# Performance work log

Hardware: AMD Instinct MI355X
Metric: run time of the kernel (lower is better)

Reference implementation:

```python
import jax, jax.numpy as jnp
import numpy as np

D_IN_NUM = 16
D_IN_CAT = 16
D_OUT = 10
DIM = 512
N_FREQ = 32
FREQ_SCALE = 0.01
D_EMB = 48
TEMP = 1.0
CHUNK = 5000


def setup_inputs() -> dict:
    key = jax.random.key(0)
    ks = jax.random.split(key, 10)
    B, N = 1024, 40000
    d_in_total = D_IN_NUM * D_EMB + D_IN_CAT
    return {
        "x_num": jax.random.uniform(ks[0], (B, D_IN_NUM), dtype=jnp.float32),
        "x_cat": jax.random.uniform(ks[1], (B, D_IN_CAT), dtype=jnp.float32),
        "y": jax.random.randint(ks[2], (B,), 0, D_OUT),
        "candidate_x_num": jax.random.uniform(ks[3], (N, D_IN_NUM), dtype=jnp.float32),
        "candidate_x_cat": jax.random.uniform(ks[4], (N, D_IN_CAT), dtype=jnp.float32),
        "candidate_y": jax.random.randint(ks[5], (N,), 0, D_OUT),
        "frequencies": FREQ_SCALE * jax.random.normal(ks[6], (D_IN_NUM, N_FREQ), dtype=jnp.float32),
        "lin_w": 0.05 * jax.random.normal(ks[7], (2 * N_FREQ, D_EMB), dtype=jnp.float32),
        "lin_b": jnp.zeros((D_EMB,), dtype=jnp.float32),
        "enc_w": 0.02 * jax.random.normal(ks[8], (d_in_total, DIM), dtype=jnp.float32),
        "enc_b": jnp.zeros((DIM,), dtype=jnp.float32),
    }


def _plr_encode(x_num, x_cat, frequencies, lin_w, lin_b, enc_w, enc_b):
    # PLR 'lite' embedding: [B, F] -> [B, F, 2*n_freq] -> [B, F, d_emb]
    t = 2.0 * jnp.pi * frequencies[None] * x_num[:, :, None]        # [B,F,n_freq]
    feats = jnp.concatenate([jnp.cos(t), jnp.sin(t)], axis=-1)       # [B,F,2n_freq]
    emb = jax.nn.relu(feats @ lin_w + lin_b)                         # [B,F,d_emb]
    flat = emb.reshape(emb.shape[0], -1)                             # [B,F*d_emb]
    h = jnp.concatenate([flat, x_cat], axis=1) @ enc_w + enc_b       # [B,dim]
    return h


def reference(x_num, x_cat, y, candidate_x_num, candidate_x_cat, candidate_y,
              frequencies, lin_w, lin_b, enc_w, enc_b):
    q = _plr_encode(x_num, x_cat, frequencies, lin_w, lin_b, enc_w, enc_b)           # [B,dim]
    c = _plr_encode(candidate_x_num, candidate_x_cat, frequencies, lin_w, lin_b, enc_w, enc_b)  # [N,dim]
    cand_y = jax.nn.one_hot(candidate_y, D_OUT, dtype=jnp.float32)                   # [N,K]

    # pairwise Euclidean distance (matmul form, as torch.cdist)
    d2 = (jnp.sum(q * q, axis=1, keepdims=True)
          + jnp.sum(c * c, axis=1)[None, :]
          - 2.0 * q @ c.T)
    dist = jnp.sqrt(jnp.maximum(d2, 1e-12)) / TEMP                                   # [B,N]
    exp_d = jnp.exp(-dist)                                                           # [B,N]

    # original accumulates per-5000-chunk logsumexp of exp(-d) additively
    B, N = exp_d.shape
    n_chunks = N // CHUNK
    lse = jax.nn.logsumexp(exp_d.reshape(B, n_chunks, CHUNK), axis=-1).sum(axis=-1)  # [B]
    logits = exp_d @ cand_y                                                          # [B,K]
    return jnp.log(logits) - lse[:, None]
```

## Files before the change

kernel.cpp:

```cpp
#include <hip/hip_runtime.h>
#include <math.h>

typedef __attribute__((ext_vector_type(8))) short bf16x8;
typedef __attribute__((ext_vector_type(4))) float f32x4;
typedef unsigned short u16;
typedef unsigned int u32;

#define BQ 1024
#define NCAND 40000
#define ROWS_TOT 41024
#define NF 16
#define NFREQ 32
#define DEMB 48
#define KDIM 800
#define ASTRIDE 808
#define DIM 512
#define NCLS 10
#define NCHUNK 8
#define CHUNKSZ 5000
#define CT_PER_CHUNK 40
#define NCT 320
#define PSTRIDE 136
#define MROWS 64
#define TWO_PI 6.28318530717958647692f

__device__ __forceinline__ u16 f2bf(float f) {
  u32 u = __float_as_uint(f);
  u32 r = u + 0x7fffu + ((u >> 16) & 1u);
  return (u16)(r >> 16);
}
__device__ __forceinline__ float bf2f(u16 b) { return __uint_as_float(((u32)b) << 16); }
__device__ __forceinline__ u32 cvt_pk_bf16(float lo, float hi) {
  u32 r;
  asm("v_cvt_pk_bf16_f32 %0, %1, %2" : "=v"(r) : "v"(lo), "v"(hi));
  return r;
}

__global__ __launch_bounds__(256)
void k_prep(const float* __restrict__ enc_w, u16* __restrict__ enc_wT)
{
  int idx = blockIdx.x * 256 + threadIdx.x;
  if (idx >= DIM * KDIM) return;
  int n = idx / KDIM, k = idx - n * KDIM;
  u16 v = 0;
  if (k < 784) v = f2bf(enc_w[k * DIM + n]);
  enc_wT[idx] = v;
}

__global__ __launch_bounds__(512, 2)
void k_encode(const float* __restrict__ xq_num, const float* __restrict__ xq_cat,
              const float* __restrict__ xc_num, const float* __restrict__ xc_cat,
              const float* __restrict__ freq, const float* __restrict__ lin_w,
              const float* __restrict__ lin_b, const u16* __restrict__ enc_wT,
              const float* __restrict__ enc_b,
              u16* __restrict__ h_bf, float* __restrict__ norms)
{
  __shared__ u16 a_s[MROWS * ASTRIDE];
  __shared__ float norm_s[MROWS];

  const int t = threadIdx.x;
  const int row0 = blockIdx.x * MROWS;
  const bool isq = (row0 < BQ);
  const float* __restrict__ xnum = isq ? xq_num : xc_num;
  const float* __restrict__ xcat = isq ? xq_cat : xc_cat;
  const int rbase = isq ? row0 : (row0 - BQ);

  const int wid = t >> 6, l = t & 63, hi = l >> 4, lo = l & 15;

  if (t < MROWS) norm_s[t] = 0.f;
  for (int i = t; i < MROWS * 16; i += 512) {
    int r = i >> 4, c = i & 15;
    a_s[r * ASTRIDE + 768 + c] = f2bf(xcat[(rbase + r) * NF + c]);
  }
  for (int i = t; i < MROWS * 24; i += 512) {
    int r = i / 24, c = i - r * 24;
    a_s[r * ASTRIDE + 784 + c] = 0;
  }

  {
    float fq[8];
    *(float4*)&fq[0] = *(const float4*)&freq[lo * NFREQ + hi * 8];
    *(float4*)&fq[4] = *(const float4*)&freq[lo * NFREQ + hi * 8 + 4];
    float xv[8];
#pragma unroll
    for (int mi = 0; mi < 8; ++mi)
      xv[mi] = xnum[(rbase + wid * 8 + mi) * NF + lo];

    bf16x8 lwb[2][3];
#pragma unroll
    for (int kf = 0; kf < 2; ++kf)
#pragma unroll
      for (int nf = 0; nf < 3; ++nf)
#pragma unroll
        for (int e = 0; e < 8; ++e)
          lwb[kf][nf][e] = (short)f2bf(lin_w[(kf * 32 + hi * 8 + e) * DEMB + nf * 16 + lo]);
    float lb[3];
#pragma unroll
    for (int nf = 0; nf < 3; ++nf) lb[nf] = lin_b[nf * 16 + lo];

#pragma unroll
    for (int mi = 0; mi < 8; ++mi) {
      bf16x8 ac, as_;
#pragma unroll
      for (int e = 0; e < 8; ++e) {
        float tt = TWO_PI * fq[e] * xv[mi];
        ac[e] = (short)f2bf(__cosf(tt));
        as_[e] = (short)f2bf(__sinf(tt));
      }
#pragma unroll
      for (int nf = 0; nf < 3; ++nf) {
        f32x4 ec = {0.f, 0.f, 0.f, 0.f};
        ec = __builtin_amdgcn_mfma_f32_16x16x32_bf16(ac, lwb[0][nf], ec, 0, 0, 0);
        ec = __builtin_amdgcn_mfma_f32_16x16x32_bf16(as_, lwb[1][nf], ec, 0, 0, 0);
#pragma unroll
        for (int reg = 0; reg < 4; ++reg) {
          int f = hi * 4 + reg;
          int r = wid * 8 + mi;
          float v = fmaxf(ec[reg] + lb[nf], 0.f);
          a_s[r * ASTRIDE + f * DEMB + nf * 16 + lo] = f2bf(v);
        }
      }
    }
  }
  __syncthreads();

  f32x4 acc[4][4];
#pragma unroll
  for (int mf = 0; mf < 4; ++mf)
#pragma unroll
    for (int nf = 0; nf < 4; ++nf) acc[mf][nf] = 0.f;

  const u16* bwbase = enc_wT + (size_t)(wid * 64 + lo) * KDIM + hi * 8;
  const u16* asbase = a_s + lo * ASTRIDE + hi * 8;

  bf16x8 afA[4], bwA[4], afB[4], bwB[4];

#define LOADK(kt, af, bw)                                                     \
  {                                                                           \
    _Pragma("unroll")                                                         \
    for (int nf = 0; nf < 4; ++nf)                                            \
      bw[nf] = *(const bf16x8*)(bwbase + (size_t)nf * 16 * KDIM + (kt) * 32); \
    _Pragma("unroll")                                                         \
    for (int mf = 0; mf < 4; ++mf)                                            \
      af[mf] = *(const bf16x8*)(asbase + mf * 16 * ASTRIDE + (kt) * 32);      \
  }
#define MFMAK(af, bw)                                                         \
  {                                                                           \
    _Pragma("unroll")                                                         \
    for (int mf = 0; mf < 4; ++mf)                                            \
      _Pragma("unroll")                                                       \
      for (int nf = 0; nf < 4; ++nf)                                          \
        acc[mf][nf] =                                                         \
            __builtin_amdgcn_mfma_f32_16x16x32_bf16(af[mf], bw[nf],           \
                                                    acc[mf][nf], 0, 0, 0);    \
  }

  LOADK(0, afA, bwA);
#pragma unroll
  for (int i = 0; i < 12; ++i) {
    LOADK(2 * i + 1, afB, bwB);
    MFMAK(afA, bwA);
    LOADK(2 * i + 2, afA, bwA);
    MFMAK(afB, bwB);
  }
  MFMAK(afA, bwA);
#undef LOADK
#undef MFMAK

  float encb_v[4];
#pragma unroll
  for (int nf = 0; nf < 4; ++nf) encb_v[nf] = enc_b[wid * 64 + nf * 16 + lo];
  float nacc[4][4];
#pragma unroll
  for (int mf = 0; mf < 4; ++mf)
#pragma unroll
    for (int r = 0; r < 4; ++r) nacc[mf][r] = 0.f;

#pragma unroll
  for (int mf = 0; mf < 4; ++mf)
#pragma unroll
    for (int nf = 0; nf < 4; ++nf)
#pragma unroll
      for (int r = 0; r < 4; ++r) {
        int m = mf * 16 + hi * 4 + r;
        int n = wid * 64 + nf * 16 + lo;
        float hv = acc[mf][nf][r] + encb_v[nf];
        u16 ub = f2bf(hv);
        h_bf[(size_t)(row0 + m) * DIM + n] = ub;
        float hb = bf2f(ub);
        nacc[mf][r] = fmaf(hb, hb, nacc[mf][r]);
      }
#pragma unroll
  for (int mf = 0; mf < 4; ++mf)
#pragma unroll
    for (int r = 0; r < 4; ++r) {
      float v = nacc[mf][r];
      v += __shfl_xor(v, 1); v += __shfl_xor(v, 2);
      v += __shfl_xor(v, 4); v += __shfl_xor(v, 8);
      if (lo == 0) atomicAdd(&norm_s[mf * 16 + hi * 4 + r], v);
    }
  __syncthreads();
  if (t < MROWS) norms[row0 + t] = norm_s[t];
}

__global__ __launch_bounds__(256)
void k_dist(const u16* __restrict__ h_bf, const float* __restrict__ norms,
            const int* __restrict__ cand_y,
            float* __restrict__ cls_part, float* __restrict__ lse_part)
{
  __shared__ __align__(16) u16 AB_s[32768];
  __shared__ float qn_s[128];
  __shared__ float cn_s[128];
  __shared__ int cy_s[128];
  __shared__ float lse_s[128];

  u16* P_s = AB_s;

  const int t = threadIdx.x;
  const int by = blockIdx.y;
  const int chunk = by / CT_PER_CHUNK;
  const int ctl = by - chunk * CT_PER_CHUNK;
  const int cand0 = chunk * CHUNKSZ + ctl * 128;
  const int cend = chunk * CHUNKSZ + CHUNKSZ;
  const int q0 = blockIdx.x * 128;

  if (t < 128) {
    lse_s[t] = 0.f;
    qn_s[t] = norms[q0 + t];
    int j = cand0 + t; if (j > cend - 1) j = cend - 1;
    cn_s[t] = norms[BQ + j];
    cy_s[t] = cand_y[j];
  }

  const int wid = t >> 6, l = t & 63, hi = l >> 4, lo = l & 15;
  const int wc = wid & 1, wq = wid >> 1;

#define STAGE(dstoff, kt)                                                      \
  {                                                                            \
    _Pragma("unroll")                                                          \
    for (int p = 0; p < 4; ++p) {                                              \
      int seg = wid * 4 + p;                                                   \
      int lrow = seg * 8 + (l >> 3);                                           \
      int scol = ((l & 7) * 16) ^ ((lrow & 7) << 4);                           \
      int crow = cand0 + lrow; if (crow > cend - 1) crow = cend - 1;           \
      const u16* srcA = h_bf + (size_t)(BQ + crow) * DIM + (kt) * 64 + (scol >> 1); \
      __builtin_amdgcn_global_load_lds(                                        \
          (const __attribute__((address_space(1))) u32*)srcA,                  \
          (__attribute__((address_space(3))) u32*)(AB_s + (dstoff) + seg * 512), \
          16, 0, 0);                                                           \
      const u16* srcB = h_bf + (size_t)(q0 + lrow) * DIM + (kt) * 64 + (scol >> 1); \
      __builtin_amdgcn_global_load_lds(                                        \
          (const __attribute__((address_space(1))) u32*)srcB,                  \
          (__attribute__((address_space(3))) u32*)(AB_s + (dstoff) + 8192 + seg * 512), \
          16, 0, 0);                                                           \
    }                                                                          \
  }

  f32x4 acc[4][4];
#pragma unroll
  for (int mi = 0; mi < 4; ++mi)
#pragma unroll
    for (int ni = 0; ni < 4; ++ni) acc[mi][ni] = 0.f;

  STAGE(0, 0);
  __syncthreads();

  int cur = 0;
  for (int kt = 0; kt < DIM / 64; ++kt) {
    if (kt < DIM / 64 - 1) STAGE((cur ^ 1) * 16384, kt + 1);
    const u16* Ac = AB_s + cur * 16384;
    const u16* Bc = Ac + 8192;
#pragma unroll
    for (int ks = 0; ks < 2; ++ks) {
      bf16x8 af[4], bq[4];
#pragma unroll
      for (int mi = 0; mi < 4; ++mi) {
        int row = wc * 64 + mi * 16 + lo;
        int byt = (hi * 16 + ks * 64) ^ ((row & 7) << 4);
        af[mi] = *(const bf16x8*)&Ac[row * 64 + (byt >> 1)];
      }
#pragma unroll
      for (int ni = 0; ni < 4; ++ni) {
        int row = wq * 64 + ni * 16 + lo;
        int byt = (hi * 16 + ks * 64) ^ ((row & 7) << 4);
        bq[ni] = *(const bf16x8*)&Bc[row * 64 + (byt >> 1)];
      }
#pragma unroll
      for (int mi = 0; mi < 4; ++mi)
#pragma unroll
        for (int ni = 0; ni < 4; ++ni)
          acc[mi][ni] = __builtin_amdgcn_mfma_f32_16x16x32_bf16(af[mi], bq[ni], acc[mi][ni], 0, 0, 0);
    }
    __syncthreads();
    cur ^= 1;
  }
#undef STAGE

  float qv[4];
#pragma unroll
  for (int ni = 0; ni < 4; ++ni) qv[ni] = qn_s[wq * 64 + ni * 16 + lo];

  u32 pk[4][4][2];
  float lacc[4] = {0.f, 0.f, 0.f, 0.f};
#pragma unroll
  for (int mi = 0; mi < 4; ++mi)
#pragma unroll
    for (int ni = 0; ni < 4; ++ni) {
      float ev[4];
#pragma unroll
      for (int r = 0; r < 4; ++r) {
        int crow = wc * 64 + mi * 16 + hi * 4 + r;
        bool valid = (cand0 + crow) < cend;
        float d2 = fmaf(-2.f, acc[mi][ni][r], cn_s[crow] + qv[ni]);
        float dist = __builtin_amdgcn_sqrtf(fmaxf(d2, 1e-12f));
        float e = valid ? __expf(-dist) : 0.f;
        ev[r] = e;
        lacc[ni] += valid ? __expf(e) : 0.f;
      }
      pk[mi][ni][0] = cvt_pk_bf16(ev[0], ev[1]);
      pk[mi][ni][1] = cvt_pk_bf16(ev[2], ev[3]);
    }

#pragma unroll
  for (int ni = 0; ni < 4; ++ni) {
    float v = lacc[ni];
    v += __shfl_xor(v, 16); v += __shfl_xor(v, 32);
    if (hi == 0) atomicAdd(&lse_s[wq * 64 + ni * 16 + lo], v);
  }

  __syncthreads();
#pragma unroll
  for (int mi = 0; mi < 4; ++mi)
#pragma unroll
    for (int ni = 0; ni < 4; ++ni) {
      int q = wq * 64 + ni * 16 + lo;
      int j0 = wc * 64 + mi * 16 + hi * 4;
      *(uint2*)&P_s[q * PSTRIDE + j0] = make_uint2(pk[mi][ni][0], pk[mi][ni][1]);
    }
  __syncthreads();

#pragma unroll
  for (int g = 0; g < 2; ++g) {
    f32x4 accc = {0.f, 0.f, 0.f, 0.f};
    const u16* Prow = P_s + (wid * 32 + g * 16 + lo) * PSTRIDE;
#pragma unroll
    for (int ks = 0; ks < 4; ++ks) {
      bf16x8 af = *(const bf16x8*)(Prow + ks * 32 + hi * 8);
      bf16x8 yb;
#pragma unroll
      for (int e = 0; e < 8; ++e) {
        int j = ks * 32 + hi * 8 + e;
        yb[e] = (short)((cy_s[j] == lo) ? 0x3F80 : 0);
      }
      accc = __builtin_amdgcn_mfma_f32_16x16x32_bf16(af, yb, accc, 0, 0, 0);
    }
    if (lo < NCLS) {
#pragma unroll
      for (int reg = 0; reg < 4; ++reg) {
        int qq = wid * 32 + g * 16 + hi * 4 + reg;
        cls_part[((size_t)by * BQ + (q0 + qq)) * NCLS + lo] = accc[reg];
      }
    }
  }

  if (t < 128) lse_part[(size_t)by * BQ + q0 + t] = lse_s[t];
}

__global__ __launch_bounds__(320)
void k_final(const float* __restrict__ cls_part, const float* __restrict__ lse_part,
             float* __restrict__ out)
{
  __shared__ float cls_sum[NCLS];
  __shared__ float ch_sum[NCHUNK];
  const int t = threadIdx.x;
  const int b = blockIdx.x;
  if (t < NCLS) cls_sum[t] = 0.f;
  if (t < NCHUNK) ch_sum[t] = 0.f;
  __syncthreads();

  float cs[NCLS];
#pragma unroll
  for (int c = 0; c < NCLS; ++c) cs[c] = cls_part[((size_t)t * BQ + b) * NCLS + c];
  float ls = lse_part[(size_t)t * BQ + b];
  atomicAdd(&ch_sum[t / CT_PER_CHUNK], ls);
#pragma unroll
  for (int c = 0; c < NCLS; ++c) {
    float w = cs[c];
    w += __shfl_xor(w, 1); w += __shfl_xor(w, 2); w += __shfl_xor(w, 4);
    w += __shfl_xor(w, 8); w += __shfl_xor(w, 16); w += __shfl_xor(w, 32);
    if ((t & 63) == 0) atomicAdd(&cls_sum[c], w);
  }
  __syncthreads();
  if (t < NCLS) {
    float lse = 0.f;
#pragma unroll
    for (int ch = 0; ch < NCHUNK; ++ch) lse += logf(ch_sum[ch]);
    out[b * NCLS + t] = logf(cls_sum[t]) - lse;
  }
}

extern "C" void kernel_launch(void* const* d_in, const int* in_sizes, int n_in,
                              void* d_out, int out_size, void* d_ws, size_t ws_size,
                              hipStream_t stream)
{
  const float* xq_num = (const float*)d_in[0];
  const float* xq_cat = (const float*)d_in[1];
  const float* xc_num = (const float*)d_in[3];
  const float* xc_cat = (const float*)d_in[4];
  const int* cand_y = (const int*)d_in[5];
  const float* freq = (const float*)d_in[6];
  const float* lin_w = (const float*)d_in[7];
  const float* lin_b = (const float*)d_in[8];
  const float* enc_w = (const float*)d_in[9];
  const float* enc_b = (const float*)d_in[10];

  u16* h_bf = (u16*)d_ws;
  float* norms = (float*)((char*)d_ws + (size_t)ROWS_TOT * DIM * 2);
  float* cls_part = norms + ROWS_TOT;
  float* lse_part = cls_part + (size_t)NCT * BQ * NCLS;
  u16* enc_wT = (u16*)(lse_part + (size_t)NCT * BQ);
  float* out = (float*)d_out;

  hipLaunchKernelGGL(k_prep, dim3((DIM * KDIM + 255) / 256), dim3(256), 0, stream,
                     enc_w, enc_wT);
  hipLaunchKernelGGL(k_encode, dim3(ROWS_TOT / MROWS), dim3(512), 0, stream,
                     xq_num, xq_cat, xc_num, xc_cat, freq, lin_w, lin_b,
                     enc_wT, enc_b, h_bf, norms);
  hipLaunchKernelGGL(k_dist, dim3(BQ / 128, NCT), dim3(256), 0, stream,
                     h_bf, norms, cand_y, cls_part, lse_part);
  hipLaunchKernelGGL(k_final, dim3(BQ), dim3(320), 0, stream,
                     cls_part, lse_part, out);
}
```

Before: 192.0 us.

## Remap k_dist blocks per XCD and prefetch two K-tiles ahead

Flattens the k_dist grid to 1D and remaps block IDs so each XCD (flat id mod 8) handles one candidate chunk with all query tiles, improving L2 locality of shared candidate and query rows. The K loop now issues two stages up front, waits with partial vmcnt counts and raw s_barrier, then refills the buffer just consumed, so loads stay in flight for a longer window. This relies on the round-robin XCD dispatch assumption and on hand-counted vmcnt values matching the number of global_load_lds issued per stage.

```diff
diff --git a/kernel.cpp b/kernel.cpp
--- a/kernel.cpp
+++ b/kernel.cpp
@@ -216,13 +216,18 @@
 
   u16* P_s = AB_s;
 
+  const int flat = blockIdx.x;
+  const int xcd = flat & 7;
+  const int i = flat >> 3;
+  const int ct = xcd * CT_PER_CHUNK + (i >> 3);
+  const int qt = i & 7;
+
   const int t = threadIdx.x;
-  const int by = blockIdx.y;
-  const int chunk = by / CT_PER_CHUNK;
-  const int ctl = by - chunk * CT_PER_CHUNK;
+  const int chunk = xcd;
+  const int ctl = ct - chunk * CT_PER_CHUNK;
   const int cand0 = chunk * CHUNKSZ + ctl * 128;
   const int cend = chunk * CHUNKSZ + CHUNKSZ;
-  const int q0 = blockIdx.x * 128;
+  const int q0 = qt * 128;
 
   if (t < 128) {
     lse_s[t] = 0.f;
@@ -263,12 +268,16 @@
     for (int ni = 0; ni < 4; ++ni) acc[mi][ni] = 0.f;
 
   STAGE(0, 0);
-  __syncthreads();
-
-  int cur = 0;
-  for (int kt = 0; kt < DIM / 64; ++kt) {
-    if (kt < DIM / 64 - 1) STAGE((cur ^ 1) * 16384, kt + 1);
-    const u16* Ac = AB_s + cur * 16384;
+  STAGE(16384, 1);
+
+#pragma unroll
+  for (int kt = 0; kt < 8; ++kt) {
+    if (kt == 7) asm volatile("s_waitcnt vmcnt(0)" ::: "memory");
+    else         asm volatile("s_waitcnt vmcnt(8)" ::: "memory");
+    __builtin_amdgcn_s_barrier();
+    __builtin_amdgcn_sched_barrier(0);
+
+    const u16* Ac = AB_s + (kt & 1) * 16384;
     const u16* Bc = Ac + 8192;
 #pragma unroll
     for (int ks = 0; ks < 2; ++ks) {
@@ -291,8 +300,9 @@
         for (int ni = 0; ni < 4; ++ni)
           acc[mi][ni] = __builtin_amdgcn_mfma_f32_16x16x32_bf16(af[mi], bq[ni], acc[mi][ni], 0, 0, 0);
     }
-    __syncthreads();
-    cur ^= 1;
+    __builtin_amdgcn_sched_barrier(0);
+    __builtin_amdgcn_s_barrier();
+    if (kt < 6) STAGE((kt & 1) * 16384, kt + 2);
   }
 #undef STAGE
 
@@ -358,12 +368,12 @@
 #pragma unroll
       for (int reg = 0; reg < 4; ++reg) {
         int qq = wid * 32 + g * 16 + hi * 4 + reg;
-        cls_part[((size_t)by * BQ + (q0 + qq)) * NCLS + lo] = accc[reg];
-      }
-    }
-  }
-
-  if (t < 128) lse_part[(size_t)by * BQ + q0 + t] = lse_s[t];
+        cls_part[((size_t)ct * BQ + (q0 + qq)) * NCLS + lo] = accc[reg];
+      }
+    }
+  }
+
+  if (t < 128) lse_part[(size_t)ct * BQ + q0 + t] = lse_s[t];
 }
 
 __global__ __launch_bounds__(320)
@@ -426,7 +436,7 @@
   hipLaunchKernelGGL(k_encode, dim3(ROWS_TOT / MROWS), dim3(512), 0, stream,
                      xq_num, xq_cat, xc_num, xc_cat, freq, lin_w, lin_b,
                      enc_wT, enc_b, h_bf, norms);
-  hipLaunchKernelGGL(k_dist, dim3(BQ / 128, NCT), dim3(256), 0, stream,
+  hipLaunchKernelGGL(k_dist, dim3(NCT * 8), dim3(256), 0, stream,
                      h_bf, norms, cand_y, cls_part, lse_part);
   hipLaunchKernelGGL(k_final, dim3(BQ), dim3(320), 0, stream,
                      cls_part, lse_part, out);
```

New measurement: 179.3 us. -6.6%, faster.
